# Kernel optimization log

Measured on AMD Instinct MI355X. Metric: run time of the kernel, lower is better.

## Reference

```python
import jax, jax.numpy as jnp
import numpy as np

V, H, B, T = 32000, 1024, 64, 512
EPS = 1e-5


def setup_inputs() -> dict:
    key = jax.random.key(0)
    ks = jax.random.split(key, 12)
    s = lambda i, shape: (jax.random.normal(ks[i], shape, dtype=jnp.float32) * 0.02)
    inp = {
        "x": jax.random.randint(ks[0], (B, T), 0, V),
        "t": jax.random.uniform(ks[1], (B,), dtype=jnp.float32),
        "emb": s(2, (V, H)),
        "w_ih1": s(3, (4 * H, H)), "w_hh1": s(4, (4 * H, H)),
        "b_ih1": jnp.zeros((4 * H,), jnp.float32), "b_hh1": jnp.zeros((4 * H,), jnp.float32),
        "gamma1": jnp.ones((H,), jnp.float32), "beta1": jnp.zeros((H,), jnp.float32),
        "w_ih2": s(5, (4 * H, H)), "w_hh2": s(6, (4 * H, H)),
        "b_ih2": jnp.zeros((4 * H,), jnp.float32), "b_hh2": jnp.zeros((4 * H,), jnp.float32),
        "gamma2": jnp.ones((H,), jnp.float32), "beta2": jnp.zeros((H,), jnp.float32),
        "fc_w": s(7, (1, H)), "fc_b": jnp.zeros((1,), jnp.float32),
        # LockedDropout: one mask per layer, reused at every timestep, pre-scaled by 1/keep
        "mask1": jax.random.bernoulli(ks[8], 0.5, (B, H)).astype(jnp.float32) / 0.5,
        "mask2": jax.random.bernoulli(ks[9], 0.7, (B, H)).astype(jnp.float32) / 0.7,
    }
    return inp


def _lstm_step(xt, h, c, w_ih, w_hh, b_ih, b_hh):
    # PyTorch LSTMCell gate order: i, f, g, o
    g = xt @ w_ih.T + h @ w_hh.T + (b_ih + b_hh)
    i, f, gg, o = jnp.split(g, 4, axis=-1)
    c = jax.nn.sigmoid(f) * c + jax.nn.sigmoid(i) * jnp.tanh(gg)
    h = jax.nn.sigmoid(o) * jnp.tanh(c)
    return h, c


def _bn(x, gamma, beta):
    # BatchNorm1d in training mode: per-feature batch stats (biased variance)
    m = x.mean(0)
    v = x.var(0)
    return gamma * (x - m) * jax.lax.rsqrt(v + EPS) + beta


def reference(x, t, emb, w_ih1, w_hh1, b_ih1, b_hh1, gamma1, beta1,
              w_ih2, w_hh2, b_ih2, b_hh2, gamma2, beta2, fc_w, fc_b,
              mask1, mask2):
    e = emb[x]                      # [B, T, H]
    e = jnp.transpose(e, (1, 0, 2)) # [T, B, H]

    def step(carry, et):
        h1, c1, h2, c2 = carry
        h1, c1 = _lstm_step(et, h1, c1, w_ih1, w_hh1, b_ih1, b_hh1)
        o = _bn(h1, gamma1, beta1) * mask1
        h2, c2 = _lstm_step(o, h2, c2, w_ih2, w_hh2, b_ih2, b_hh2)
        o = _bn(h2, gamma2, beta2) * mask2
        return (h1, c1, h2, c2), o

    z = jnp.zeros((B, H), jnp.float32)
    _, outs = jax.lax.scan(step, (z, z, z, z), e)  # outs: [T, B, H]

    pooled = outs.max(axis=0)                      # MaxPool1d over time -> [B, H]
    logits = (pooled @ fc_w.T + fc_b)[:, 0]        # [B]
    # BCEWithLogitsLoss (mean), numerically stable
    loss = jnp.mean(jnp.maximum(logits, 0.0) - logits * t + jnp.log1p(jnp.exp(-jnp.abs(logits))))
    return (loss, logits)
```

## Files before the change

### kernel.cpp

```cpp
#include <hip/hip_runtime.h>

#define HDIM  1024
#define BDIM  64
#define TDIM  512
#define FRAGB 131072
#define FRAGE 65536
#define WPAD  1048
#define SLOTS 4
#define NGRP  8

typedef __bf16 bf16x8 __attribute__((ext_vector_type(8)));
typedef float  f32x4  __attribute__((ext_vector_type(4)));
typedef int    i32x4  __attribute__((ext_vector_type(4)));

#define MFMA(a, b, c) __builtin_amdgcn_mfma_f32_16x16x32_bf16(a, b, c, 0, 0, 0)

#define GL(dst, p, off) \
    asm volatile("global_load_dwordx4 %0, %1, off offset:" off " sc0 sc1" \
                 : "=v"(dst) : "v"(p) : "memory")
#define GLF16(f, p) do { \
    const char* p0_ = (const char*)(p); \
    const char* p1_ = p0_ + 4096; const char* p2_ = p0_ + 8192; const char* p3_ = p0_ + 12288; \
    GL(f[0],  p0_, "0"); GL(f[1],  p0_, "1024"); GL(f[2],  p0_, "2048"); GL(f[3],  p0_, "3072"); \
    GL(f[4],  p1_, "0"); GL(f[5],  p1_, "1024"); GL(f[6],  p1_, "2048"); GL(f[7],  p1_, "3072"); \
    GL(f[8],  p2_, "0"); GL(f[9],  p2_, "1024"); GL(f[10], p2_, "2048"); GL(f[11], p2_, "3072"); \
    GL(f[12], p3_, "0"); GL(f[13], p3_, "1024"); GL(f[14], p3_, "2048"); GL(f[15], p3_, "3072"); \
} while (0)
#define WAITV() asm volatile("s_waitcnt vmcnt(0)" ::: "memory")
#define GS16(p, v) \
    asm volatile("global_store_dwordx4 %0, %1, off sc0 sc1" :: "v"(p), "v"(v) : "memory")

__device__ __forceinline__ float sigf(float x) { return 1.0f / (1.0f + expf(-x)); }

__device__ __forceinline__ bf16x8 cvt8(const float* p) {
    const f32x4* q = (const f32x4*)p;
    f32x4 a = q[0], b = q[1];
    bf16x8 r;
    r[0] = (__bf16)a[0]; r[1] = (__bf16)a[1]; r[2] = (__bf16)a[2]; r[3] = (__bf16)a[3];
    r[4] = (__bf16)b[0]; r[5] = (__bf16)b[1]; r[6] = (__bf16)b[2]; r[7] = (__bf16)b[3];
    return r;
}

__device__ __forceinline__ void wspin(const int* base) {
    int l = threadIdx.x & 63;
    const int* p = (l < 8) ? base + l * 16 : nullptr;
    for (;;) {
        int v = p ? __hip_atomic_load(p, __ATOMIC_RELAXED, __HIP_MEMORY_SCOPE_AGENT) : 16;
        if (__all(v >= 16)) break;
        __builtin_amdgcn_s_sleep(1);
    }
}
__device__ __forceinline__ void spin1(const int* c, int n) {
    if (threadIdx.x == 0)
        while (__hip_atomic_load(c, __ATOMIC_RELAXED, __HIP_MEMORY_SCOPE_AGENT) < n)
            __builtin_amdgcn_s_sleep(1);
    __syncthreads();
}

__device__ __forceinline__ void gemm16(const char* pa, const __bf16* bw0, const __bf16* bw1,
                                       f32x4& c00, f32x4& c01, f32x4& c10, f32x4& c11) {
#pragma unroll
    for (int i = 0; i < 16; i++) {
        bf16x8 a0v = *(const bf16x8*)(pa + i * 1024);
        bf16x8 a1v = *(const bf16x8*)(pa + 32768 + i * 1024);
        bf16x8 w0  = *(const bf16x8*)(bw0 + i * 32);
        bf16x8 w1  = *(const bf16x8*)(bw1 + i * 32);
        c00 = MFMA(a0v, w0, c00); c01 = MFMA(a0v, w1, c01);
        c10 = MFMA(a1v, w0, c10); c11 = MFMA(a1v, w1, c11);
    }
}
__device__ __forceinline__ void gemm16s(const bf16x8* f0, const bf16x8* f1,
                                        const __bf16* bw0, const __bf16* bw1,
                                        f32x4& c00, f32x4& c01, f32x4& c10, f32x4& c11) {
#pragma unroll
    for (int i = 0; i < 16; i++) {
        bf16x8 w0 = *(const bf16x8*)(bw0 + i * 32);
        bf16x8 w1 = *(const bf16x8*)(bw1 + i * 32);
        c00 = MFMA(f0[i], w0, c00); c01 = MFMA(f0[i], w1, c01);
        c10 = MFMA(f1[i], w0, c10); c11 = MFMA(f1[i], w1, c11);
    }
}

__global__ void gather_emb(const int* __restrict__ x, const float* __restrict__ emb,
                           __bf16* __restrict__ xseqfrag) {
    int t = blockIdx.x;
    for (int u = threadIdx.x; u < 8192; u += 256) {
        int lane = u & 63, c = (u >> 6) & 31, bt = u >> 11;
        int row = lane & 15, quad = lane >> 4;
        int b = bt * 16 + row, k = c * 32 + quad * 8;
        int tok = x[b * TDIM + t];
        bf16x8 r = cvt8(emb + (size_t)tok * HDIM + k);
        *(bf16x8*)(xseqfrag + (size_t)t * FRAGE + (size_t)u * 8) = r;
    }
}

template <int BIG>
__global__ void __launch_bounds__(512, 1) rnn_all(
    const int* __restrict__ x, const float* __restrict__ tv,
    const float* __restrict__ emb,
    const float* __restrict__ w_ih1, const float* __restrict__ w_hh1,
    const float* __restrict__ b_ih1, const float* __restrict__ b_hh1,
    const float* __restrict__ gamma1, const float* __restrict__ beta1,
    const float* __restrict__ w_ih2, const float* __restrict__ w_hh2,
    const float* __restrict__ b_ih2, const float* __restrict__ b_hh2,
    const float* __restrict__ gamma2, const float* __restrict__ beta2,
    const float* __restrict__ fc_w, const float* __restrict__ fc_b,
    const float* __restrict__ mask1, const float* __restrict__ mask2,
    const __bf16* __restrict__ xseq, int use_xseq,
    int* __restrict__ l1h, int* __restrict__ l1o, int* __restrict__ l2h,
    int* __restrict__ poolg, const char* __restrict__ hzero,
    char* __restrict__ h1p, char* __restrict__ h2p, char* __restrict__ o1p,
    float* __restrict__ pooled, float* __restrict__ out) {
    __shared__ __bf16 wih_s[32 * WPAD];
    __shared__ __bf16 whh_s[32 * WPAD];
    __shared__ float bias_s[32];
    __shared__ float gbufX[32 * 68];
    __shared__ float gbufH[32 * 68];
    __shared__ float xh[8 * 68];
    __shared__ float stat_m[8], stat_r[8];
    __shared__ __align__(16) __bf16 hstage[512];
    __shared__ __align__(16) __bf16 ostage[512];

    const int tid   = threadIdx.x;
    const int layer = blockIdx.x & 1;
    const int lb    = blockIdx.x >> 1;
    const int grp   = lb >> 4;
    const int fbase = lb * 8;

    const float* w_ih = layer ? w_ih2 : w_ih1;
    const float* w_hh = layer ? w_hh2 : w_hh1;
    const float* b_ih = layer ? b_ih2 : b_ih1;
    const float* b_hh = layer ? b_hh2 : b_hh1;
    const float* gam_ = layer ? gamma2 : gamma1;
    const float* bet_ = layer ? beta2  : beta1;
    const float* msk_ = layer ? mask2  : mask1;

    for (int idx = tid; idx < 32 * HDIM; idx += 512) {
        int n = idx >> 10, k = idx & 1023;
        int row = (n >> 3) * HDIM + fbase + (n & 7);
        wih_s[n * WPAD + k] = (__bf16)w_ih[row * HDIM + k];
        whh_s[n * WPAD + k] = (__bf16)w_hh[row * HDIM + k];
    }
    if (tid < 32) {
        int row = (tid >> 3) * HDIM + fbase + (tid & 7);
        bias_s[tid] = b_ih[row] + b_hh[row];
    }
    __syncthreads();
    if (BIG)
        __builtin_amdgcn_fence(__ATOMIC_ACQUIRE, "agent");

    const int lane = tid & 63;
    const int wv   = tid >> 6;
    const int bh   = wv & 1;
    const int kh   = (wv >> 1) & 1;
    const int g    = wv >> 2;
    const int qm   = lane & 15;
    const int quad = lane >> 4;
    const int aoff = (bh * 64 + kh * 16) * 1024 + lane * 16;

    const __bf16* bw0 = (g ? whh_s : wih_s) + qm * WPAD + kh * 512 + quad * 8;
    const __bf16* bw1 = bw0 + 16 * WPAD;

    const int bb = tid >> 3, jj = tid & 7;
    const int feat = fbase + jj;
    const float gv = gam_[feat], bev = bet_[feat], mv = msk_[bb * HDIM + feat];
    float cst = 0.0f, pmax = -1e30f;

    const int soff = (((lane >> 4) * 32 + (lb >> 2)) * 64 + ((lb & 3) * 16 + (lane & 15))) * 16;

    char* h_self = layer ? h2p : h1p;
    int*  ch     = layer ? l2h : l1h;

#pragma unroll 1
    for (int t = 0; t < TDIM; t++) {
        f32x4 a00 = {0.f,0.f,0.f,0.f}, a01 = {0.f,0.f,0.f,0.f};
        f32x4 a10 = {0.f,0.f,0.f,0.f}, a11 = {0.f,0.f,0.f,0.f};

        if (g == 0) {
            if (layer == 0) {
                if (use_xseq) {
                    gemm16((const char*)xseq + (size_t)t * FRAGB + aoff, bw0, bw1,
                           a00, a01, a10, a11);
                } else {
                    const float* pe0 = emb + (size_t)x[(bh*32 + qm)*TDIM + t]*HDIM + kh*512 + quad*8;
                    const float* pe1 = emb + (size_t)x[(bh*32 + 16 + qm)*TDIM + t]*HDIM + kh*512 + quad*8;
#pragma unroll 4
                    for (int i = 0; i < 16; i++) {
                        bf16x8 v0 = cvt8(pe0 + i * 32), v1 = cvt8(pe1 + i * 32);
                        bf16x8 w0 = *(const bf16x8*)(bw0 + i * 32);
                        bf16x8 w1 = *(const bf16x8*)(bw1 + i * 32);
                        a00 = MFMA(v0, w0, a00); a01 = MFMA(v0, w1, a01);
                        a10 = MFMA(v1, w0, a10); a11 = MFMA(v1, w1, a11);
                    }
                }
            } else {
                wspin(l1o + (size_t)t * NGRP * 16);
                if (BIG) {
                    gemm16(o1p + (size_t)t * FRAGB + aoff, bw0, bw1, a00, a01, a10, a11);
                } else {
                    bf16x8 f0[16], f1[16];
                    const char* p = o1p + (size_t)(t & (SLOTS - 1)) * FRAGB + aoff;
                    GLF16(f0, p); GLF16(f1, p + 32768); WAITV();
                    gemm16s(f0, f1, bw0, bw1, a00, a01, a10, a11);
                }
            }
        } else {
            if (t >= 1) wspin(ch + (size_t)(t - 1) * NGRP * 16);
            if (BIG) {
                const char* src = (t == 0) ? hzero : (const char*)(h_self + (size_t)(t - 1) * FRAGB);
                gemm16(src + aoff, bw0, bw1, a00, a01, a10, a11);
            } else {
                bf16x8 f0[16], f1[16];
                const char* p = h_self + (size_t)(t & 1) * FRAGB + aoff;
                GLF16(f0, p); GLF16(f1, p + 32768); WAITV();
                gemm16s(f0, f1, bw0, bw1, a00, a01, a10, a11);
            }
        }

        float* myg = g ? gbufH : gbufX;
        const int r0  = bh * 32 + quad * 4;
        const int i00 = qm * 68 + r0, i01 = (16 + qm) * 68 + r0;
        if (kh == 0) {
            if (!g) {
                float b0 = bias_s[qm], b1 = bias_s[16 + qm];
                f32x4 s0 = {b0, b0, b0, b0}, s1 = {b1, b1, b1, b1};
                a00 += s0; a01 += s1; a10 += s0; a11 += s1;
            }
            *(f32x4*)&myg[i00]      = a00;
            *(f32x4*)&myg[i01]      = a01;
            *(f32x4*)&myg[i00 + 16] = a10;
            *(f32x4*)&myg[i01 + 16] = a11;
        }
        __syncthreads();
        if (kh == 1) {
            f32x4 v;
            v = *(const f32x4*)&myg[i00];      v += a00; *(f32x4*)&myg[i00]      = v;
            v = *(const f32x4*)&myg[i01];      v += a01; *(f32x4*)&myg[i01]      = v;
            v = *(const f32x4*)&myg[i00 + 16]; v += a10; *(f32x4*)&myg[i00 + 16] = v;
            v = *(const f32x4*)&myg[i01 + 16]; v += a11; *(f32x4*)&myg[i01 + 16] = v;
        }
        __syncthreads();

        const int cb = jj * 68 + bb;
        float gi = gbufX[cb]          + gbufH[cb];
        float gf = gbufX[cb + 8*68]   + gbufH[cb + 8*68];
        float gg = gbufX[cb + 16*68]  + gbufH[cb + 16*68];
        float go = gbufX[cb + 24*68]  + gbufH[cb + 24*68];
        cst = sigf(gf) * cst + sigf(gi) * tanhf(gg);
        float h = sigf(go) * tanhf(cst);
        hstage[tid] = (__bf16)h;
        xh[jj * 68 + bb] = h;
        __syncthreads();

        size_t hslot = BIG ? (size_t)t * FRAGB : (size_t)((t + 1) & 1) * FRAGB;
        if (wv == 0) {
            i32x4 val = *(const i32x4*)(hstage + lane * 8);
            GS16(h_self + hslot + soff, val);
        }
        float v = xh[wv * 68 + lane];
        float s1 = v, s2 = v * v;
#pragma unroll
        for (int off = 32; off; off >>= 1) {
            s1 += __shfl_xor(s1, off);
            s2 += __shfl_xor(s2, off);
        }
        if (lane == 0) {
            float m  = s1 * (1.0f / 64.0f);
            float va = s2 * (1.0f / 64.0f) - m * m;
            stat_m[wv] = m;
            stat_r[wv] = rsqrtf(va + 1e-5f);
        }
        if (wv == 0) {
            WAITV();
            if (lane == 0)
                __hip_atomic_fetch_add(ch + ((size_t)t * NGRP + grp) * 16, 1,
                                       __ATOMIC_RELAXED, __HIP_MEMORY_SCOPE_AGENT);
        }
        __syncthreads();

        float o = ((h - stat_m[jj]) * stat_r[jj] * gv + bev) * mv;
        if (layer == 0) {
            ostage[tid] = (__bf16)o;
            __syncthreads();
            if (wv == 1) {
                if (!BIG && t >= SLOTS)
                    wspin(l2h + (size_t)(t - SLOTS) * NGRP * 16);
                i32x4 val = *(const i32x4*)(ostage + lane * 8);
                size_t oslot = BIG ? (size_t)t * FRAGB : (size_t)(t & (SLOTS - 1)) * FRAGB;
                GS16(o1p + oslot + soff, val);
                WAITV();
                if (lane == 0)
                    __hip_atomic_fetch_add(l1o + ((size_t)t * NGRP + grp) * 16, 1,
                                           __ATOMIC_RELAXED, __HIP_MEMORY_SCOPE_AGENT);
            }
        } else {
            pmax = fmaxf(pmax, o);
        }
    }

    if (layer == 1) {
        __hip_atomic_store(&pooled[bb * HDIM + feat], pmax,
                           __ATOMIC_RELAXED, __HIP_MEMORY_SCOPE_AGENT);
        WAITV();
        __syncthreads();
        if (tid == 0)
            __hip_atomic_fetch_add(poolg, 1, __ATOMIC_RELAXED, __HIP_MEMORY_SCOPE_AGENT);

        if (lb == 0) {
            spin1(poolg, 128);
            __builtin_amdgcn_fence(__ATOMIC_ACQUIRE, "agent");
            int b  = wv * 8 + (lane >> 3);
            int l8 = lane & 7;
            float s = 0.0f;
            for (int f = l8 * 128; f < l8 * 128 + 128; f++)
                s += pooled[b * HDIM + f] * fc_w[f];
            s += __shfl_xor(s, 1); s += __shfl_xor(s, 2); s += __shfl_xor(s, 4);
            float logit = s + fc_b[0];
            if (l8 == 0) {
                out[1 + b] = logit;
                gbufX[b] = fmaxf(logit, 0.0f) - logit * tv[b] + log1pf(expf(-fabsf(logit)));
            }
            __syncthreads();
            if (tid < 64) {
                float term = gbufX[tid];
#pragma unroll
                for (int off = 32; off; off >>= 1) term += __shfl_xor(term, off);
                if (tid == 0) out[0] = term * (1.0f / 64.0f);
            }
        }
    }
}

extern "C" void kernel_launch(void* const* d_in, const int* in_sizes, int n_in,
                              void* d_out, int out_size, void* d_ws, size_t ws_size,
                              hipStream_t stream) {
    const int*   x    = (const int*)d_in[0];
    const float* tv   = (const float*)d_in[1];
    const float* emb  = (const float*)d_in[2];
    const float* wih1 = (const float*)d_in[3];
    const float* whh1 = (const float*)d_in[4];
    const float* bih1 = (const float*)d_in[5];
    const float* bhh1 = (const float*)d_in[6];
    const float* g1   = (const float*)d_in[7];
    const float* be1  = (const float*)d_in[8];
    const float* wih2 = (const float*)d_in[9];
    const float* whh2 = (const float*)d_in[10];
    const float* bih2 = (const float*)d_in[11];
    const float* bhh2 = (const float*)d_in[12];
    const float* g2   = (const float*)d_in[13];
    const float* be2  = (const float*)d_in[14];
    const float* fcw  = (const float*)d_in[15];
    const float* fcb  = (const float*)d_in[16];
    const float* m1   = (const float*)d_in[17];
    const float* m2   = (const float*)d_in[18];

    char* w = (char*)d_ws;
    float* out = (float*)d_out;

    const size_t SEQB = (size_t)TDIM * FRAGB;
    size_t boff = 0;
    int*   B_l1h   = (int*)(w + boff); boff += 262144;
    int*   B_l1o   = (int*)(w + boff); boff += 262144;
    int*   B_l2h   = (int*)(w + boff); boff += 262144;
    int*   B_poolg = (int*)(w + boff); boff += 4096;
    char*  B_hzero = w + boff;         boff += FRAGB;
    size_t B_msz   = boff;
    char*  B_h1    = w + boff;         boff += SEQB;
    char*  B_h2    = w + boff;         boff += SEQB;
    char*  B_o1    = w + boff;         boff += SEQB;
    float* B_pool  = (float*)(w + boff); boff += 262144;
    __bf16* B_xseq = (__bf16*)(w + boff); boff += SEQB;
    size_t need_big = boff;

    if (ws_size >= need_big) {
        hipMemsetAsync(d_ws, 0, B_msz, stream);
        gather_emb<<<dim3(TDIM), dim3(256), 0, stream>>>(x, emb, B_xseq);
        int use_xseq = 1;
        void* args[] = {&x, &tv, &emb, &wih1, &whh1, &bih1, &bhh1, &g1, &be1,
                        &wih2, &whh2, &bih2, &bhh2, &g2, &be2, &fcw, &fcb, &m1, &m2,
                        (void*)&B_xseq, &use_xseq,
                        &B_l1h, &B_l1o, &B_l2h, &B_poolg, (void*)&B_hzero,
                        &B_h1, &B_h2, &B_o1, &B_pool, &out};
        hipLaunchCooperativeKernel((void*)rnn_all<1>, dim3(256), dim3(512), args, 0, stream);
        return;
    }

    int*    l1h    = (int*)(w);
    int*    l1o    = (int*)(w + 262144);
    int*    l2h    = (int*)(w + 524288);
    int*    poolg  = (int*)(w + 786432);
    char*   hzero  = w;
    char*   h1frag = w + 790528;
    char*   h2frag = h1frag + 262144;
    char*   o1frag = h2frag + 262144;
    float*  pooled = (float*)(o1frag + 524288);
    __bf16* xseq   = (__bf16*)((char*)pooled + 262144);
    size_t fixed   = (size_t)((char*)xseq - w);
    int use_xseq = (ws_size >= fixed + SEQB) ? 1 : 0;

    hipMemsetAsync(d_ws, 0, fixed, stream);
    if (use_xseq)
        gather_emb<<<dim3(TDIM), dim3(256), 0, stream>>>(x, emb, xseq);

    void* args[] = {&x, &tv, &emb, &wih1, &whh1, &bih1, &bhh1, &g1, &be1,
                    &wih2, &whh2, &bih2, &bhh2, &g2, &be2, &fcw, &fcb, &m1, &m2,
                    (void*)&xseq, &use_xseq,
                    &l1h, &l1o, &l2h, &poolg, (void*)&hzero,
                    &h1frag, &h2frag, &o1frag, &pooled, &out};
    hipLaunchCooperativeKernel((void*)rnn_all<0>, dim3(256), dim3(512), args, 0, stream);
}
```

Measured before the change: 3.908 ms.

## Keep LSTM weight slices in registers and split gate reduction buffers

Each thread now holds its recurrent and input weight fragments in VGPRs (32 bf16x8 vectors) for the whole run instead of reading them from padded LDS each step. This frees about 134 KB of LDS, and the launch bound is raised to 2 blocks per CU. The two K-halves now write to separate gate buffers, which removes one barrier and the read-modify-write pass. Sigmoid and tanh use hardware exp2/rcp intrinsics. The risks are heavy register pressure from 128 weight VGPRs plus fragment buffers, possible spills under the 2-block launch bound, and slightly lower activation accuracy.

```diff
diff --git a/kernel.cpp b/kernel.cpp
--- a/kernel.cpp
+++ b/kernel.cpp
@@ -5,7 +5,6 @@
 #define TDIM  512
 #define FRAGB 131072
 #define FRAGE 65536
-#define WPAD  1048
 #define SLOTS 4
 #define NGRP  8
 
@@ -30,7 +29,12 @@
 #define GS16(p, v) \
     asm volatile("global_store_dwordx4 %0, %1, off sc0 sc1" :: "v"(p), "v"(v) : "memory")
 
-__device__ __forceinline__ float sigf(float x) { return 1.0f / (1.0f + expf(-x)); }
+__device__ __forceinline__ float sigf(float x) {
+    return __builtin_amdgcn_rcpf(1.0f + __builtin_amdgcn_exp2f(-1.44269504f * x));
+}
+__device__ __forceinline__ float tanh_fast(float x) {
+    return 2.0f * __builtin_amdgcn_rcpf(1.0f + __builtin_amdgcn_exp2f(-2.88539008f * x)) - 1.0f;
+}
 
 __device__ __forceinline__ bf16x8 cvt8(const float* p) {
     const f32x4* q = (const f32x4*)p;
@@ -57,27 +61,15 @@
     __syncthreads();
 }
 
-__device__ __forceinline__ void gemm16(const char* pa, const __bf16* bw0, const __bf16* bw1,
-                                       f32x4& c00, f32x4& c01, f32x4& c10, f32x4& c11) {
+__device__ __forceinline__ void gemm16r(const char* pa,
+                                        const bf16x8 (&w0)[16], const bf16x8 (&w1)[16],
+                                        f32x4& c00, f32x4& c01, f32x4& c10, f32x4& c11) {
 #pragma unroll
     for (int i = 0; i < 16; i++) {
         bf16x8 a0v = *(const bf16x8*)(pa + i * 1024);
         bf16x8 a1v = *(const bf16x8*)(pa + 32768 + i * 1024);
-        bf16x8 w0  = *(const bf16x8*)(bw0 + i * 32);
-        bf16x8 w1  = *(const bf16x8*)(bw1 + i * 32);
-        c00 = MFMA(a0v, w0, c00); c01 = MFMA(a0v, w1, c01);
-        c10 = MFMA(a1v, w0, c10); c11 = MFMA(a1v, w1, c11);
-    }
-}
-__device__ __forceinline__ void gemm16s(const bf16x8* f0, const bf16x8* f1,
-                                        const __bf16* bw0, const __bf16* bw1,
-                                        f32x4& c00, f32x4& c01, f32x4& c10, f32x4& c11) {
-#pragma unroll
-    for (int i = 0; i < 16; i++) {
-        bf16x8 w0 = *(const bf16x8*)(bw0 + i * 32);
-        bf16x8 w1 = *(const bf16x8*)(bw1 + i * 32);
-        c00 = MFMA(f0[i], w0, c00); c01 = MFMA(f0[i], w1, c01);
-        c10 = MFMA(f1[i], w0, c10); c11 = MFMA(f1[i], w1, c11);
+        c00 = MFMA(a0v, w0[i], c00); c01 = MFMA(a0v, w1[i], c01);
+        c10 = MFMA(a1v, w0[i], c10); c11 = MFMA(a1v, w1[i], c11);
     }
 }
 
@@ -95,7 +87,7 @@
 }
 
 template <int BIG>
-__global__ void __launch_bounds__(512, 1) rnn_all(
+__global__ void __launch_bounds__(512, 2) rnn_all(
     const int* __restrict__ x, const float* __restrict__ tv,
     const float* __restrict__ emb,
     const float* __restrict__ w_ih1, const float* __restrict__ w_hh1,
@@ -111,11 +103,11 @@
     int* __restrict__ poolg, const char* __restrict__ hzero,
     char* __restrict__ h1p, char* __restrict__ h2p, char* __restrict__ o1p,
     float* __restrict__ pooled, float* __restrict__ out) {
-    __shared__ __bf16 wih_s[32 * WPAD];
-    __shared__ __bf16 whh_s[32 * WPAD];
     __shared__ float bias_s[32];
-    __shared__ float gbufX[32 * 68];
-    __shared__ float gbufH[32 * 68];
+    __shared__ float gbufX0[32 * 68];
+    __shared__ float gbufX1[32 * 68];
+    __shared__ float gbufH0[32 * 68];
+    __shared__ float gbufH1[32 * 68];
     __shared__ float xh[8 * 68];
     __shared__ float stat_m[8], stat_r[8];
     __shared__ __align__(16) __bf16 hstage[512];
@@ -135,12 +127,6 @@
     const float* bet_ = layer ? beta2  : beta1;
     const float* msk_ = layer ? mask2  : mask1;
 
-    for (int idx = tid; idx < 32 * HDIM; idx += 512) {
-        int n = idx >> 10, k = idx & 1023;
-        int row = (n >> 3) * HDIM + fbase + (n & 7);
-        wih_s[n * WPAD + k] = (__bf16)w_ih[row * HDIM + k];
-        whh_s[n * WPAD + k] = (__bf16)w_hh[row * HDIM + k];
-    }
     if (tid < 32) {
         int row = (tid >> 3) * HDIM + fbase + (tid & 7);
         bias_s[tid] = b_ih[row] + b_hh[row];
@@ -158,8 +144,19 @@
     const int quad = lane >> 4;
     const int aoff = (bh * 64 + kh * 16) * 1024 + lane * 16;
 
-    const __bf16* bw0 = (g ? whh_s : wih_s) + qm * WPAD + kh * 512 + quad * 8;
-    const __bf16* bw1 = bw0 + 16 * WPAD;
+    bf16x8 wr0[16], wr1[16];
+    {
+        const float* wsrc = g ? w_hh : w_ih;
+        const float* p0 = wsrc + (size_t)((qm >> 3) * HDIM + fbase + (qm & 7)) * HDIM
+                               + kh * 512 + quad * 8;
+        const float* p1 = wsrc + (size_t)(((16 + qm) >> 3) * HDIM + fbase + (qm & 7)) * HDIM
+                               + kh * 512 + quad * 8;
+#pragma unroll
+        for (int i = 0; i < 16; i++) {
+            wr0[i] = cvt8(p0 + i * 32);
+            wr1[i] = cvt8(p1 + i * 32);
+        }
+    }
 
     const int bb = tid >> 3, jj = tid & 7;
     const int feat = fbase + jj;
@@ -179,75 +176,79 @@
         if (g == 0) {
             if (layer == 0) {
                 if (use_xseq) {
-                    gemm16((const char*)xseq + (size_t)t * FRAGB + aoff, bw0, bw1,
-                           a00, a01, a10, a11);
+                    gemm16r((const char*)xseq + (size_t)t * FRAGB + aoff, wr0, wr1,
+                            a00, a01, a10, a11);
                 } else {
                     const float* pe0 = emb + (size_t)x[(bh*32 + qm)*TDIM + t]*HDIM + kh*512 + quad*8;
                     const float* pe1 = emb + (size_t)x[(bh*32 + 16 + qm)*TDIM + t]*HDIM + kh*512 + quad*8;
 #pragma unroll 4
                     for (int i = 0; i < 16; i++) {
                         bf16x8 v0 = cvt8(pe0 + i * 32), v1 = cvt8(pe1 + i * 32);
-                        bf16x8 w0 = *(const bf16x8*)(bw0 + i * 32);
-                        bf16x8 w1 = *(const bf16x8*)(bw1 + i * 32);
-                        a00 = MFMA(v0, w0, a00); a01 = MFMA(v0, w1, a01);
-                        a10 = MFMA(v1, w0, a10); a11 = MFMA(v1, w1, a11);
+                        a00 = MFMA(v0, wr0[i], a00); a01 = MFMA(v0, wr1[i], a01);
+                        a10 = MFMA(v1, wr0[i], a10); a11 = MFMA(v1, wr1[i], a11);
                     }
                 }
             } else {
                 wspin(l1o + (size_t)t * NGRP * 16);
                 if (BIG) {
-                    gemm16(o1p + (size_t)t * FRAGB + aoff, bw0, bw1, a00, a01, a10, a11);
+                    gemm16r(o1p + (size_t)t * FRAGB + aoff, wr0, wr1, a00, a01, a10, a11);
                 } else {
-                    bf16x8 f0[16], f1[16];
                     const char* p = o1p + (size_t)(t & (SLOTS - 1)) * FRAGB + aoff;
-                    GLF16(f0, p); GLF16(f1, p + 32768); WAITV();
-                    gemm16s(f0, f1, bw0, bw1, a00, a01, a10, a11);
+                    bf16x8 f[16];
+                    GLF16(f, p); WAITV();
+#pragma unroll
+                    for (int i = 0; i < 16; i++) {
+                        a00 = MFMA(f[i], wr0[i], a00); a01 = MFMA(f[i], wr1[i], a01);
+                    }
+                    GLF16(f, p + 32768); WAITV();
+#pragma unroll
+                    for (int i = 0; i < 16; i++) {
+                        a10 = MFMA(f[i], wr0[i], a10); a11 = MFMA(f[i], wr1[i], a11);
+                    }
                 }
             }
         } else {
             if (t >= 1) wspin(ch + (size_t)(t - 1) * NGRP * 16);
             if (BIG) {
                 const char* src = (t == 0) ? hzero : (const char*)(h_self + (size_t)(t - 1) * FRAGB);
-                gemm16(src + aoff, bw0, bw1, a00, a01, a10, a11);
+                gemm16r(src + aoff, wr0, wr1, a00, a01, a10, a11);
             } else {
-                bf16x8 f0[16], f1[16];
                 const char* p = h_self + (size_t)(t & 1) * FRAGB + aoff;
-                GLF16(f0, p); GLF16(f1, p + 32768); WAITV();
-                gemm16s(f0, f1, bw0, bw1, a00, a01, a10, a11);
+                bf16x8 f[16];
+                GLF16(f, p); WAITV();
+#pragma unroll
+                for (int i = 0; i < 16; i++) {
+                    a00 = MFMA(f[i], wr0[i], a00); a01 = MFMA(f[i], wr1[i], a01);
+                }
+                GLF16(f, p + 32768); WAITV();
+#pragma unroll
+                for (int i = 0; i < 16; i++) {
+                    a10 = MFMA(f[i], wr0[i], a10); a11 = MFMA(f[i], wr1[i], a11);
+                }
             }
         }
 
-        float* myg = g ? gbufH : gbufX;
+        float* myg = g ? (kh ? gbufH1 : gbufH0) : (kh ? gbufX1 : gbufX0);
         const int r0  = bh * 32 + quad * 4;
         const int i00 = qm * 68 + r0, i01 = (16 + qm) * 68 + r0;
-        if (kh == 0) {
-            if (!g) {
-                float b0 = bias_s[qm], b1 = bias_s[16 + qm];
-                f32x4 s0 = {b0, b0, b0, b0}, s1 = {b1, b1, b1, b1};
-                a00 += s0; a01 += s1; a10 += s0; a11 += s1;
-            }
-            *(f32x4*)&myg[i00]      = a00;
-            *(f32x4*)&myg[i01]      = a01;
-            *(f32x4*)&myg[i00 + 16] = a10;
-            *(f32x4*)&myg[i01 + 16] = a11;
-        }
+        if (!g && !kh) {
+            float b0 = bias_s[qm], b1 = bias_s[16 + qm];
+            f32x4 s0 = {b0, b0, b0, b0}, s1 = {b1, b1, b1, b1};
+            a00 += s0; a01 += s1; a10 += s0; a11 += s1;
+        }
+        *(f32x4*)&myg[i00]      = a00;
+        *(f32x4*)&myg[i01]      = a01;
+        *(f32x4*)&myg[i00 + 16] = a10;
+        *(f32x4*)&myg[i01 + 16] = a11;
         __syncthreads();
-        if (kh == 1) {
-            f32x4 v;
-            v = *(const f32x4*)&myg[i00];      v += a00; *(f32x4*)&myg[i00]      = v;
-            v = *(const f32x4*)&myg[i01];      v += a01; *(f32x4*)&myg[i01]      = v;
-            v = *(const f32x4*)&myg[i00 + 16]; v += a10; *(f32x4*)&myg[i00 + 16] = v;
-            v = *(const f32x4*)&myg[i01 + 16]; v += a11; *(f32x4*)&myg[i01 + 16] = v;
-        }
-        __syncthreads();
 
         const int cb = jj * 68 + bb;
-        float gi = gbufX[cb]          + gbufH[cb];
-        float gf = gbufX[cb + 8*68]   + gbufH[cb + 8*68];
-        float gg = gbufX[cb + 16*68]  + gbufH[cb + 16*68];
-        float go = gbufX[cb + 24*68]  + gbufH[cb + 24*68];
-        cst = sigf(gf) * cst + sigf(gi) * tanhf(gg);
-        float h = sigf(go) * tanhf(cst);
+        float gi = gbufX0[cb] + gbufX1[cb] + gbufH0[cb] + gbufH1[cb];
+        float gf = gbufX0[cb + 8*68] + gbufX1[cb + 8*68] + gbufH0[cb + 8*68] + gbufH1[cb + 8*68];
+        float gg = gbufX0[cb + 16*68] + gbufX1[cb + 16*68] + gbufH0[cb + 16*68] + gbufH1[cb + 16*68];
+        float go = gbufX0[cb + 24*68] + gbufX1[cb + 24*68] + gbufH0[cb + 24*68] + gbufH1[cb + 24*68];
+        cst = sigf(gf) * cst + sigf(gi) * tanh_fast(gg);
+        float h = sigf(go) * tanh_fast(cst);
         hstage[tid] = (__bf16)h;
         xh[jj * 68 + bb] = h;
         __syncthreads();
@@ -318,11 +319,11 @@
             float logit = s + fc_b[0];
             if (l8 == 0) {
                 out[1 + b] = logit;
-                gbufX[b] = fmaxf(logit, 0.0f) - logit * tv[b] + log1pf(expf(-fabsf(logit)));
+                gbufX0[b] = fmaxf(logit, 0.0f) - logit * tv[b] + log1pf(expf(-fabsf(logit)));
             }
             __syncthreads();
             if (tid < 64) {
-                float term = gbufX[tid];
+                float term = gbufX0[tid];
 #pragma unroll
                 for (int off = 32; off; off >>= 1) term += __shfl_xor(term, off);
                 if (tid == 0) out[0] = term * (1.0f / 64.0f);
```

Measured after the change: 3.767 ms. 1.04x faster.
